# Kernel optimization log

Measured on AMD Instinct MI355X. Metric: run time of the kernel, lower is better.

The kernel has to match this reference:

```python
import jax, jax.numpy as jnp
import numpy as np

SLIDING_WINDOW = 4
M = 450

def setup_inputs() -> dict:
    P, C, d = 256, 128, 128
    key = jax.random.key(0)
    ks = jax.random.split(key, 16)
    n = lambda k, shape: jax.random.normal(k, shape, dtype=jnp.float32)
    # Linear init scale ~ 1/sqrt(fan_in) to keep activations sane
    s_m = 1.0 / np.sqrt(M)
    return {
        "x": n(ks[0], (8, P, C)),
        "t": 8,
        "TwE": n(ks[1], (SLIDING_WINDOW, d)),
        "PE": n(ks[2], (P, d)),
        "CE": n(ks[3], (C, d)),
        "mE": n(ks[4], (M, d)),
        "ext_W1": n(ks[5], (M, M)) * s_m,
        "ext_b1": n(ks[6], (M,)) * s_m,
        "ext_W2": n(ks[7], (M, M)) * s_m,
        "ext_b2": n(ks[8], (M,)) * s_m,
        "dec_W1": n(ks[9], (M, M)) * s_m,
        "dec_b1": n(ks[10], (M,)) * s_m,
        "dec_W2": n(ks[11], (4 * P * C, M)) * s_m,
        "dec_b2": n(ks[12], (4 * P * C,)) * s_m,
    }

def reference(x, t, TwE, PE, CE, mE, ext_W1, ext_b1, ext_W2, ext_b2,
              dec_W1, dec_b1, dec_W2, dec_b2):
    P, C = PE.shape[0], CE.shape[0]
    xw = x[-SLIDING_WINDOW:]  # (4, P, C)
    # Factorized CP contraction: identical math to
    # einsum('ti,pi,ci,mi->tpcm') followed by einsum('tpcm,tpc->m'),
    # but reduces over t,p,c first without materializing the rank-4 tensor.
    f = jnp.einsum('tpc,ti,pi,ci->i', xw, TwE, PE, CE)  # (d,)
    feat = mE @ f  # (m,)
    # extractor_MLP: Linear(m,m) -> ReLU -> Linear(m,m)
    feat = ext_W2 @ jax.nn.relu(ext_W1 @ feat + ext_b1) + ext_b2
    # dec: Linear(m,m) -> ReLU -> Linear(m, 4*P*C)
    out = dec_W2 @ jax.nn.relu(dec_W1 @ feat + dec_b1) + dec_b2
    return out.reshape(4, P, C)
```

## Files before the change

### kernel.cpp

```cpp
#include <hip/hip_runtime.h>

typedef float vf4 __attribute__((ext_vector_type(4)));

#define WS_FPART 0
#define WS_H1    640
#define WS_FEAT  1152
#define WS_H2    1664

__global__ __launch_bounds__(256) void k_f(
    const float* __restrict__ x, const float* __restrict__ TwE,
    const float* __restrict__ PE, const float* __restrict__ CE,
    float* __restrict__ fpart) {
  const int i = blockIdx.x >> 2;
  const int t = blockIdx.x & 3;
  const int tid = threadIdx.x;
  __shared__ float sCE[128];
  __shared__ float coef[256];
  __shared__ float red[4];
  const float tw = TwE[t * 128 + i];
  if (tid < 128) sCE[tid] = CE[tid * 128 + i];
  coef[tid] = tw * PE[tid * 128 + i];
  __syncthreads();
  const int lane = tid & 63;
  const int wv = tid >> 6;
  const float2 ce = ((const float2*)sCE)[lane];
  const float2* Xw = (const float2*)(x + 4 * 256 * 128);
  float acc = 0.f;
  const int l0 = wv * 64;
#pragma unroll 8
  for (int k = 0; k < 64; ++k) {
    int l = l0 + k;
    int q = (t << 8) + l;
    float2 v = Xw[q * 64 + lane];
    acc += coef[l] * (v.x * ce.x + v.y * ce.y);
  }
#pragma unroll
  for (int off = 32; off > 0; off >>= 1) acc += __shfl_down(acc, off);
  if (lane == 0) red[wv] = acc;
  __syncthreads();
  if (tid == 0) fpart[t * 128 + i] = red[0] + red[1] + red[2] + red[3];
}

__global__ __launch_bounds__(256) void k_h1(
    const float* __restrict__ fpart, const float* __restrict__ mE,
    const float* __restrict__ eW1, const float* __restrict__ eb1,
    float* __restrict__ h1) {
  __shared__ float sf[128];
  __shared__ float sfeat0[450];
  const int tid = threadIdx.x;
  if (tid < 128)
    sf[tid] = (fpart[tid] + fpart[128 + tid]) + (fpart[256 + tid] + fpart[384 + tid]);
  __syncthreads();
  for (int r = tid; r < 450; r += 256) {
    const float4* row = (const float4*)(mE + r * 128);
    float a0 = 0.f, a1 = 0.f, a2 = 0.f, a3 = 0.f;
#pragma unroll 8
    for (int k = 0; k < 32; ++k) {
      float4 m = row[k];
      a0 += m.x * sf[4 * k];
      a1 += m.y * sf[4 * k + 1];
      a2 += m.z * sf[4 * k + 2];
      a3 += m.w * sf[4 * k + 3];
    }
    sfeat0[r] = (a0 + a1) + (a2 + a3);
  }
  __syncthreads();
  const int lane = tid & 63;
  const int row = blockIdx.x * 4 + (tid >> 6);
  if (row < 450) {
    const float2* Wr = (const float2*)(eW1 + row * 450);
    float acc = 0.f;
#pragma unroll
    for (int k = 0; k < 4; ++k) {
      int idx = lane + (k << 6);
      if (idx < 225) {
        float2 w = Wr[idx];
        acc += w.x * sfeat0[2 * idx] + w.y * sfeat0[2 * idx + 1];
      }
    }
#pragma unroll
    for (int off = 32; off > 0; off >>= 1) acc += __shfl_down(acc, off);
    if (lane == 0) h1[row] = fmaxf(acc + eb1[row], 0.f);
  }
}

__global__ __launch_bounds__(256) void k_mv450(
    const float* __restrict__ W, const float* __restrict__ b,
    const float* __restrict__ vin, float* __restrict__ vout, int relu) {
  __shared__ float sv[450];
  const int tid = threadIdx.x;
  if (tid < 450) sv[tid] = vin[tid];
  if (tid + 256 < 450) sv[tid + 256] = vin[tid + 256];
  __syncthreads();
  const int lane = tid & 63;
  const int row = blockIdx.x * 4 + (tid >> 6);
  if (row >= 450) return;
  const float2* Wr = (const float2*)(W + row * 450);
  float acc = 0.f;
#pragma unroll
  for (int k = 0; k < 4; ++k) {
    int idx = lane + (k << 6);
    if (idx < 225) {
      float2 w = Wr[idx];
      acc += w.x * sv[2 * idx] + w.y * sv[2 * idx + 1];
    }
  }
#pragma unroll
  for (int off = 32; off > 0; off >>= 1) acc += __shfl_down(acc, off);
  if (lane == 0) {
    float r = acc + b[row];
    if (relu) r = fmaxf(r, 0.f);
    vout[row] = r;
  }
}

__global__ __launch_bounds__(512) void k_dec2(
    const float* __restrict__ W, const float* __restrict__ b,
    const float* __restrict__ h, float* __restrict__ out) {
  __shared__ float sv2[900];
  const int tid = threadIdx.x;
  for (int k = tid; k < 900; k += 512) sv2[k] = h[k < 450 ? k : k - 450];
  __syncthreads();
  const int lane = tid & 63;
  const int rp = blockIdx.x * 8 + (tid >> 6);
  const vf4* Wp = (const vf4*)(W + (size_t)rp * 900);
  float accA = 0.f, accB = 0.f;
#pragma unroll
  for (int k = 0; k < 3; ++k) {
    int j = lane + (k << 6);
    vf4 w = __builtin_nontemporal_load(&Wp[j]);
    const float* s = &sv2[4 * j];
    float p01 = w.x * s[0] + w.y * s[1];
    float p23 = w.z * s[2] + w.w * s[3];
    if (4 * j + 3 < 450)      accA += p01 + p23;
    else if (4 * j >= 450)    accB += p01 + p23;
    else { accA += p01; accB += p23; }
  }
  if (lane < 33) {
    int j = 192 + lane;
    vf4 w = __builtin_nontemporal_load(&Wp[j]);
    const float* s = &sv2[4 * j];
    accB += w.x * s[0] + w.y * s[1] + w.z * s[2] + w.w * s[3];
  }
#pragma unroll
  for (int off = 32; off > 0; off >>= 1) {
    accA += __shfl_down(accA, off);
    accB += __shfl_down(accB, off);
  }
  if (lane == 0) {
    int r = rp * 2;
    __builtin_nontemporal_store(accA + b[r],     &out[r]);
    __builtin_nontemporal_store(accB + b[r + 1], &out[r + 1]);
  }
}

extern "C" void kernel_launch(void* const* d_in, const int* in_sizes, int n_in,
                              void* d_out, int out_size, void* d_ws, size_t ws_size,
                              hipStream_t stream) {
  const float* x   = (const float*)d_in[0];
  const float* TwE = (const float*)d_in[2];
  const float* PE  = (const float*)d_in[3];
  const float* CE  = (const float*)d_in[4];
  const float* mE  = (const float*)d_in[5];
  const float* eW1 = (const float*)d_in[6];
  const float* eb1 = (const float*)d_in[7];
  const float* eW2 = (const float*)d_in[8];
  const float* eb2 = (const float*)d_in[9];
  const float* dW1 = (const float*)d_in[10];
  const float* db1 = (const float*)d_in[11];
  const float* dW2 = (const float*)d_in[12];
  const float* db2 = (const float*)d_in[13];
  float* out = (float*)d_out;
  float* ws  = (float*)d_ws;

  k_f    <<<512,  256, 0, stream>>>(x, TwE, PE, CE, ws + WS_FPART);
  k_h1   <<<113,  256, 0, stream>>>(ws + WS_FPART, mE, eW1, eb1, ws + WS_H1);
  k_mv450<<<113,  256, 0, stream>>>(eW2, eb2, ws + WS_H1, ws + WS_FEAT, 0);
  k_mv450<<<113,  256, 0, stream>>>(dW1, db1, ws + WS_FEAT, ws + WS_H2, 1);
  k_dec2 <<<8192, 512, 0, stream>>>(dW2, db2, ws + WS_H2, out);
}
```

Baseline: 358.2 us.

## Fuse front-end MLP kernels into one persistent kernel with grid barriers

Merges the four small front-end kernels (CP contraction, mE projection plus first extractor layer, second extractor layer, first decoder layer) into one 512-block kernel separated by atomic-counter grid barriers. A memset now resets the counter each call. The aim is to cut kernel launch gaps and tail latency between the tiny serial matvecs. It depends on all 512 blocks being co-resident, which launch_bounds(256,2) is meant to allow, or the barrier deadlocks. It also swaps the nontemporal loads of dW2 in the big decoder kernel for ordinary loads.

```diff
diff --git a/kernel.cpp b/kernel.cpp
--- a/kernel.cpp
+++ b/kernel.cpp
@@ -2,115 +2,160 @@
 
 typedef float vf4 __attribute__((ext_vector_type(4)));
 
-#define WS_FPART 0
-#define WS_H1    640
-#define WS_FEAT  1152
-#define WS_H2    1664
-
-__global__ __launch_bounds__(256) void k_f(
+#define WS_FPART 16
+#define WS_H1    528
+#define WS_FEAT  1040
+#define WS_H2    1552
+
+#define NBLK 512
+#define NACT 113
+
+__device__ __forceinline__ void gbar(unsigned* ctr, unsigned target) {
+  __syncthreads();
+  if (threadIdx.x == 0) {
+    __hip_atomic_fetch_add(ctr, 1u, __ATOMIC_ACQ_REL, __HIP_MEMORY_SCOPE_AGENT);
+    while (__hip_atomic_load(ctr, __ATOMIC_ACQUIRE, __HIP_MEMORY_SCOPE_AGENT) < target)
+      __builtin_amdgcn_s_sleep(2);
+  }
+  __syncthreads();
+}
+
+__device__ __forceinline__ float aload(const float* p) {
+  return __hip_atomic_load(p, __ATOMIC_RELAXED, __HIP_MEMORY_SCOPE_AGENT);
+}
+__device__ __forceinline__ void astore(float* p, float v) {
+  __hip_atomic_store(p, v, __ATOMIC_RELAXED, __HIP_MEMORY_SCOPE_AGENT);
+}
+
+__global__ __launch_bounds__(256, 2) void k_front(
     const float* __restrict__ x, const float* __restrict__ TwE,
     const float* __restrict__ PE, const float* __restrict__ CE,
-    float* __restrict__ fpart) {
-  const int i = blockIdx.x >> 2;
-  const int t = blockIdx.x & 3;
-  const int tid = threadIdx.x;
+    const float* __restrict__ mE,
+    const float* __restrict__ eW1, const float* __restrict__ eb1,
+    const float* __restrict__ eW2, const float* __restrict__ eb2,
+    const float* __restrict__ dW1, const float* __restrict__ db1,
+    unsigned* __restrict__ bar, float* __restrict__ ws) {
+  float* fpart = ws + WS_FPART;
+  float* h1    = ws + WS_H1;
+  float* feat  = ws + WS_FEAT;
+  float* h2    = ws + WS_H2;
+  const int tid  = threadIdx.x;
+  const int b    = blockIdx.x;
+  const int lane = tid & 63;
+  const int wv   = tid >> 6;
+
   __shared__ float sCE[128];
   __shared__ float coef[256];
   __shared__ float red[4];
-  const float tw = TwE[t * 128 + i];
-  if (tid < 128) sCE[tid] = CE[tid * 128 + i];
-  coef[tid] = tw * PE[tid * 128 + i];
-  __syncthreads();
-  const int lane = tid & 63;
-  const int wv = tid >> 6;
-  const float2 ce = ((const float2*)sCE)[lane];
-  const float2* Xw = (const float2*)(x + 4 * 256 * 128);
-  float acc = 0.f;
-  const int l0 = wv * 64;
+  __shared__ float svec[450];
+  __shared__ float sfeat0[450];
+
+  {
+    const int i = b >> 2;
+    const int t = b & 3;
+    const float tw = TwE[t * 128 + i];
+    if (tid < 128) sCE[tid] = CE[tid * 128 + i];
+    coef[tid] = tw * PE[tid * 128 + i];
+    __syncthreads();
+    const float2 ce = ((const float2*)sCE)[lane];
+    const float2* Xw = (const float2*)(x + 4 * 256 * 128);
+    float acc = 0.f;
+    const int l0 = wv * 64;
 #pragma unroll 8
-  for (int k = 0; k < 64; ++k) {
-    int l = l0 + k;
-    int q = (t << 8) + l;
-    float2 v = Xw[q * 64 + lane];
-    acc += coef[l] * (v.x * ce.x + v.y * ce.y);
-  }
-#pragma unroll
-  for (int off = 32; off > 0; off >>= 1) acc += __shfl_down(acc, off);
-  if (lane == 0) red[wv] = acc;
-  __syncthreads();
-  if (tid == 0) fpart[t * 128 + i] = red[0] + red[1] + red[2] + red[3];
-}
-
-__global__ __launch_bounds__(256) void k_h1(
-    const float* __restrict__ fpart, const float* __restrict__ mE,
-    const float* __restrict__ eW1, const float* __restrict__ eb1,
-    float* __restrict__ h1) {
-  __shared__ float sf[128];
-  __shared__ float sfeat0[450];
-  const int tid = threadIdx.x;
-  if (tid < 128)
-    sf[tid] = (fpart[tid] + fpart[128 + tid]) + (fpart[256 + tid] + fpart[384 + tid]);
-  __syncthreads();
-  for (int r = tid; r < 450; r += 256) {
-    const float4* row = (const float4*)(mE + r * 128);
-    float a0 = 0.f, a1 = 0.f, a2 = 0.f, a3 = 0.f;
+    for (int k = 0; k < 64; ++k) {
+      int l = l0 + k;
+      int q = (t << 8) + l;
+      float2 v = Xw[q * 64 + lane];
+      acc += coef[l] * (v.x * ce.x + v.y * ce.y);
+    }
+#pragma unroll
+    for (int off = 32; off > 0; off >>= 1) acc += __shfl_down(acc, off);
+    if (lane == 0) red[wv] = acc;
+    __syncthreads();
+    if (tid == 0) astore(&fpart[t * 128 + i], red[0] + red[1] + red[2] + red[3]);
+  }
+  gbar(bar, NBLK);
+
+  const int row = b * 4 + wv;
+
+  if (b < NACT) {
+    if (tid < 128)
+      svec[tid] = (aload(&fpart[tid]) + aload(&fpart[128 + tid]))
+                + (aload(&fpart[256 + tid]) + aload(&fpart[384 + tid]));
+    __syncthreads();
+    for (int r = tid; r < 450; r += 256) {
+      const float4* mrow = (const float4*)(mE + r * 128);
+      float a0 = 0.f, a1 = 0.f, a2 = 0.f, a3 = 0.f;
 #pragma unroll 8
-    for (int k = 0; k < 32; ++k) {
-      float4 m = row[k];
-      a0 += m.x * sf[4 * k];
-      a1 += m.y * sf[4 * k + 1];
-      a2 += m.z * sf[4 * k + 2];
-      a3 += m.w * sf[4 * k + 3];
-    }
-    sfeat0[r] = (a0 + a1) + (a2 + a3);
-  }
-  __syncthreads();
-  const int lane = tid & 63;
-  const int row = blockIdx.x * 4 + (tid >> 6);
-  if (row < 450) {
-    const float2* Wr = (const float2*)(eW1 + row * 450);
-    float acc = 0.f;
-#pragma unroll
-    for (int k = 0; k < 4; ++k) {
-      int idx = lane + (k << 6);
-      if (idx < 225) {
-        float2 w = Wr[idx];
-        acc += w.x * sfeat0[2 * idx] + w.y * sfeat0[2 * idx + 1];
-      }
-    }
-#pragma unroll
-    for (int off = 32; off > 0; off >>= 1) acc += __shfl_down(acc, off);
-    if (lane == 0) h1[row] = fmaxf(acc + eb1[row], 0.f);
-  }
-}
-
-__global__ __launch_bounds__(256) void k_mv450(
-    const float* __restrict__ W, const float* __restrict__ b,
-    const float* __restrict__ vin, float* __restrict__ vout, int relu) {
-  __shared__ float sv[450];
-  const int tid = threadIdx.x;
-  if (tid < 450) sv[tid] = vin[tid];
-  if (tid + 256 < 450) sv[tid + 256] = vin[tid + 256];
-  __syncthreads();
-  const int lane = tid & 63;
-  const int row = blockIdx.x * 4 + (tid >> 6);
-  if (row >= 450) return;
-  const float2* Wr = (const float2*)(W + row * 450);
-  float acc = 0.f;
-#pragma unroll
-  for (int k = 0; k < 4; ++k) {
-    int idx = lane + (k << 6);
-    if (idx < 225) {
-      float2 w = Wr[idx];
-      acc += w.x * sv[2 * idx] + w.y * sv[2 * idx + 1];
-    }
-  }
-#pragma unroll
-  for (int off = 32; off > 0; off >>= 1) acc += __shfl_down(acc, off);
-  if (lane == 0) {
-    float r = acc + b[row];
-    if (relu) r = fmaxf(r, 0.f);
-    vout[row] = r;
+      for (int k = 0; k < 32; ++k) {
+        float4 m = mrow[k];
+        a0 += m.x * svec[4 * k];
+        a1 += m.y * svec[4 * k + 1];
+        a2 += m.z * svec[4 * k + 2];
+        a3 += m.w * svec[4 * k + 3];
+      }
+      sfeat0[r] = (a0 + a1) + (a2 + a3);
+    }
+    __syncthreads();
+    if (row < 450) {
+      const float2* Wr = (const float2*)(eW1 + row * 450);
+      float acc = 0.f;
+#pragma unroll
+      for (int k = 0; k < 4; ++k) {
+        int idx = lane + (k << 6);
+        if (idx < 225) {
+          float2 w = Wr[idx];
+          acc += w.x * sfeat0[2 * idx] + w.y * sfeat0[2 * idx + 1];
+        }
+      }
+#pragma unroll
+      for (int off = 32; off > 0; off >>= 1) acc += __shfl_down(acc, off);
+      if (lane == 0) astore(&h1[row], fmaxf(acc + eb1[row], 0.f));
+    }
+  }
+  gbar(bar, 2 * NBLK);
+
+  if (b < NACT) {
+    if (tid < 450) svec[tid] = aload(&h1[tid]);
+    if (tid + 256 < 450) svec[tid + 256] = aload(&h1[tid + 256]);
+    __syncthreads();
+    if (row < 450) {
+      const float2* Wr = (const float2*)(eW2 + row * 450);
+      float acc = 0.f;
+#pragma unroll
+      for (int k = 0; k < 4; ++k) {
+        int idx = lane + (k << 6);
+        if (idx < 225) {
+          float2 w = Wr[idx];
+          acc += w.x * svec[2 * idx] + w.y * svec[2 * idx + 1];
+        }
+      }
+#pragma unroll
+      for (int off = 32; off > 0; off >>= 1) acc += __shfl_down(acc, off);
+      if (lane == 0) astore(&feat[row], acc + eb2[row]);
+    }
+  }
+  gbar(bar, 3 * NBLK);
+
+  if (b < NACT) {
+    if (tid < 450) svec[tid] = aload(&feat[tid]);
+    if (tid + 256 < 450) svec[tid + 256] = aload(&feat[tid + 256]);
+    __syncthreads();
+    if (row < 450) {
+      const float2* Wr = (const float2*)(dW1 + row * 450);
+      float acc = 0.f;
+#pragma unroll
+      for (int k = 0; k < 4; ++k) {
+        int idx = lane + (k << 6);
+        if (idx < 225) {
+          float2 w = Wr[idx];
+          acc += w.x * svec[2 * idx] + w.y * svec[2 * idx + 1];
+        }
+      }
+#pragma unroll
+      for (int off = 32; off > 0; off >>= 1) acc += __shfl_down(acc, off);
+      if (lane == 0) astore(&h2[row], fmaxf(acc + db1[row], 0.f));
+    }
   }
 }
 
@@ -128,7 +173,7 @@
 #pragma unroll
   for (int k = 0; k < 3; ++k) {
     int j = lane + (k << 6);
-    vf4 w = __builtin_nontemporal_load(&Wp[j]);
+    vf4 w = Wp[j];
     const float* s = &sv2[4 * j];
     float p01 = w.x * s[0] + w.y * s[1];
     float p23 = w.z * s[2] + w.w * s[3];
@@ -138,7 +183,7 @@
   }
   if (lane < 33) {
     int j = 192 + lane;
-    vf4 w = __builtin_nontemporal_load(&Wp[j]);
+    vf4 w = Wp[j];
     const float* s = &sv2[4 * j];
     accB += w.x * s[0] + w.y * s[1] + w.z * s[2] + w.w * s[3];
   }
@@ -172,10 +217,10 @@
   const float* db2 = (const float*)d_in[13];
   float* out = (float*)d_out;
   float* ws  = (float*)d_ws;
-
-  k_f    <<<512,  256, 0, stream>>>(x, TwE, PE, CE, ws + WS_FPART);
-  k_h1   <<<113,  256, 0, stream>>>(ws + WS_FPART, mE, eW1, eb1, ws + WS_H1);
-  k_mv450<<<113,  256, 0, stream>>>(eW2, eb2, ws + WS_H1, ws + WS_FEAT, 0);
-  k_mv450<<<113,  256, 0, stream>>>(dW1, db1, ws + WS_FEAT, ws + WS_H2, 1);
+  unsigned* bar = (unsigned*)d_ws;
+
+  hipMemsetAsync(d_ws, 0, 16, stream);
+  k_front<<<NBLK, 256, 0, stream>>>(x, TwE, PE, CE, mE,
+                                    eW1, eb1, eW2, eb2, dW1, db1, bar, ws);
   k_dec2 <<<8192, 512, 0, stream>>>(dW2, db2, ws + WS_H2, out);
 }
```

Result: slower. 482.2 us (+34.6%).

## Fuse extractor MLP and first decoder layer into one kernel with redundant compute

Applied to the files above, without the earlier changes.

Merges the three small 450x450 matvec kernels into a single kernel, cutting two launches and two global round-trips for intermediate vectors. Each of the 113 blocks redundantly computes both extractor layers in full using one thread per output row, then does its slice of the decoder's first layer. This removes inter-kernel gaps, but every block now runs long serial per-thread dot products with uncoalesced row-wise weight reads. That could lengthen the critical path before the large final decoder kernel.

```diff
diff --git a/kernel.cpp b/kernel.cpp
--- a/kernel.cpp
+++ b/kernel.cpp
@@ -3,9 +3,7 @@
 typedef float vf4 __attribute__((ext_vector_type(4)));
 
 #define WS_FPART 0
-#define WS_H1    640
-#define WS_FEAT  1152
-#define WS_H2    1664
+#define WS_H2    512
 
 __global__ __launch_bounds__(256) void k_f(
     const float* __restrict__ x, const float* __restrict__ TwE,
@@ -41,12 +39,16 @@
   if (tid == 0) fpart[t * 128 + i] = red[0] + red[1] + red[2] + red[3];
 }
 
-__global__ __launch_bounds__(256) void k_h1(
+__global__ __launch_bounds__(256) void k_rest(
     const float* __restrict__ fpart, const float* __restrict__ mE,
     const float* __restrict__ eW1, const float* __restrict__ eb1,
-    float* __restrict__ h1) {
+    const float* __restrict__ eW2, const float* __restrict__ eb2,
+    const float* __restrict__ dW1, const float* __restrict__ db1,
+    float* __restrict__ h2) {
   __shared__ float sf[128];
   __shared__ float sfeat0[450];
+  __shared__ float sh1[450];
+  __shared__ float sfeat[450];
   const int tid = threadIdx.x;
   if (tid < 128)
     sf[tid] = (fpart[tid] + fpart[128 + tid]) + (fpart[256 + tid] + fpart[384 + tid]);
@@ -65,52 +67,46 @@
     sfeat0[r] = (a0 + a1) + (a2 + a3);
   }
   __syncthreads();
+  for (int r = tid; r < 450; r += 256) {
+    const float2* row = (const float2*)(eW1 + r * 450);
+    float a0 = 0.f, a1 = 0.f;
+#pragma unroll 5
+    for (int k = 0; k < 225; ++k) {
+      float2 w = row[k];
+      a0 += w.x * sfeat0[2 * k];
+      a1 += w.y * sfeat0[2 * k + 1];
+    }
+    sh1[r] = fmaxf(a0 + a1 + eb1[r], 0.f);
+  }
+  __syncthreads();
+  for (int r = tid; r < 450; r += 256) {
+    const float2* row = (const float2*)(eW2 + r * 450);
+    float a0 = 0.f, a1 = 0.f;
+#pragma unroll 5
+    for (int k = 0; k < 225; ++k) {
+      float2 w = row[k];
+      a0 += w.x * sh1[2 * k];
+      a1 += w.y * sh1[2 * k + 1];
+    }
+    sfeat[r] = a0 + a1 + eb2[r];
+  }
+  __syncthreads();
   const int lane = tid & 63;
   const int row = blockIdx.x * 4 + (tid >> 6);
   if (row < 450) {
-    const float2* Wr = (const float2*)(eW1 + row * 450);
+    const float2* Wr = (const float2*)(dW1 + row * 450);
     float acc = 0.f;
 #pragma unroll
     for (int k = 0; k < 4; ++k) {
       int idx = lane + (k << 6);
       if (idx < 225) {
         float2 w = Wr[idx];
-        acc += w.x * sfeat0[2 * idx] + w.y * sfeat0[2 * idx + 1];
+        acc += w.x * sfeat[2 * idx] + w.y * sfeat[2 * idx + 1];
       }
     }
 #pragma unroll
     for (int off = 32; off > 0; off >>= 1) acc += __shfl_down(acc, off);
-    if (lane == 0) h1[row] = fmaxf(acc + eb1[row], 0.f);
-  }
-}
-
-__global__ __launch_bounds__(256) void k_mv450(
-    const float* __restrict__ W, const float* __restrict__ b,
-    const float* __restrict__ vin, float* __restrict__ vout, int relu) {
-  __shared__ float sv[450];
-  const int tid = threadIdx.x;
-  if (tid < 450) sv[tid] = vin[tid];
-  if (tid + 256 < 450) sv[tid + 256] = vin[tid + 256];
-  __syncthreads();
-  const int lane = tid & 63;
-  const int row = blockIdx.x * 4 + (tid >> 6);
-  if (row >= 450) return;
-  const float2* Wr = (const float2*)(W + row * 450);
-  float acc = 0.f;
-#pragma unroll
-  for (int k = 0; k < 4; ++k) {
-    int idx = lane + (k << 6);
-    if (idx < 225) {
-      float2 w = Wr[idx];
-      acc += w.x * sv[2 * idx] + w.y * sv[2 * idx + 1];
-    }
-  }
-#pragma unroll
-  for (int off = 32; off > 0; off >>= 1) acc += __shfl_down(acc, off);
-  if (lane == 0) {
-    float r = acc + b[row];
-    if (relu) r = fmaxf(r, 0.f);
-    vout[row] = r;
+    if (lane == 0) h2[row] = fmaxf(acc + db1[row], 0.f);
   }
 }
 
@@ -173,9 +169,8 @@
   float* out = (float*)d_out;
   float* ws  = (float*)d_ws;
 
-  k_f    <<<512,  256, 0, stream>>>(x, TwE, PE, CE, ws + WS_FPART);
-  k_h1   <<<113,  256, 0, stream>>>(ws + WS_FPART, mE, eW1, eb1, ws + WS_H1);
-  k_mv450<<<113,  256, 0, stream>>>(eW2, eb2, ws + WS_H1, ws + WS_FEAT, 0);
-  k_mv450<<<113,  256, 0, stream>>>(dW1, db1, ws + WS_FEAT, ws + WS_H2, 1);
-  k_dec2 <<<8192, 512, 0, stream>>>(dW2, db2, ws + WS_H2, out);
+  k_f   <<<512,  256, 0, stream>>>(x, TwE, PE, CE, ws + WS_FPART);
+  k_rest<<<113,  256, 0, stream>>>(ws + WS_FPART, mE, eW1, eb1, eW2, eb2,
+                                   dW1, db1, ws + WS_H2);
+  k_dec2<<<8192, 512, 0, stream>>>(dW2, db2, ws + WS_H2, out);
 }
```

Result: slower. 442.0 us (+23.4%).
